# Kernel optimization log

Measured on AMD Instinct MI355X. Metric: run time of the kernel, lower is better.

The kernel has to match this reference:

```python
import jax, jax.numpy as jnp
import numpy as np
from jax import lax

H = 64      # hidden_size
VOC = 512   # num_embedding
L = 2       # num_layers


def layernorm(x, g, b, eps=1e-5):
    mu = jnp.mean(x, axis=-1, keepdims=True)
    var = jnp.mean((x - mu) ** 2, axis=-1, keepdims=True)
    return (x - mu) * lax.rsqrt(var + eps) * g + b


def conv3d(x, w, b):
    # x: [B, U, V, W, Cin] (channels-last), w: [3,3,3,Cin,Cout]
    return lax.conv_general_dilated(
        x, w, (1, 1, 1), 'SAME',
        dimension_numbers=('NDHWC', 'DHWIO', 'NDHWC')) + b


def setup_inputs() -> dict:
    key = jax.random.key(0)
    ks = jax.random.split(key, 8)
    f = lambda k, s, sc: jax.random.normal(k, s, jnp.float32) * sc
    return {
        'code': jax.random.randint(ks[0], (2, 5, 1, 8, 8, 8), 0, VOC),
        'ncode': jax.random.randint(ks[1], (2, 3, 1, 8, 8, 8), 0, VOC),
        'emb': f(ks[2], (VOC, H), 0.02),
        'win': f(ks[3], (L, 3, 3, 3, H, 4 * H), 0.05),
        'bin_': jnp.zeros((L, 4 * H), jnp.float32),
        'gin_w': jnp.ones((L, 4 * H), jnp.float32),
        'gin_b': jnp.zeros((L, 4 * H), jnp.float32),
        'wh': f(ks[4], (L, 3, 3, 3, H, 4 * H), 0.05),
        'bh': jnp.zeros((L, 4 * H), jnp.float32),
        'gh_w': jnp.ones((L, 4 * H), jnp.float32),
        'gh_b': jnp.zeros((L, 4 * H), jnp.float32),
        'w1': f(ks[5], (H, H), 0.05),
        'b1': jnp.zeros((H,), jnp.float32),
        'ln_g': jnp.ones((H,), jnp.float32),
        'ln_b': jnp.zeros((H,), jnp.float32),
        'w2': f(ks[6], (H, VOC), 0.05),
        'b2': jnp.zeros((VOC,), jnp.float32),
    }


def _forward(code, ncode, emb, win, bin_, gin_w, gin_b, wh, bh, gh_w, gh_b,
             w1, b1, ln_g, ln_b, w2, b2):
    N, Sn, C, U, V, W = ncode.shape
    x = jnp.concatenate([code, ncode[:, :-1]], axis=1)  # [N,S,C,U,V,W]
    S = x.shape[1]
    x = jnp.transpose(x, (0, 2, 1, 3, 4, 5)).reshape(N * C, S, U, V, W)
    h = emb[x]  # [NC, S, U, V, W, H]
    Hd = h.shape[-1]
    for i in range(L):
        # input-path conv is recurrence-free: batch it over all timesteps
        gi = layernorm(conv3d(h.reshape(N * C * S, U, V, W, Hd), win[i], bin_[i]),
                       gin_w[i], gin_b[i])
        gi = jnp.moveaxis(gi.reshape(N * C, S, U, V, W, 4 * Hd), 1, 0)  # [S,NC,U,V,W,4H]

        def step(carry, g, i=i):
            hx, cx = carry
            gates = g + layernorm(conv3d(hx, wh[i], bh[i]), gh_w[i], gh_b[i])
            ig, fg, cg, og = jnp.split(gates, 4, axis=-1)
            cx = jax.nn.sigmoid(fg) * cx + jax.nn.sigmoid(ig) * jnp.tanh(cg)
            hx = jax.nn.sigmoid(og) * jnp.tanh(cx)
            return (hx, cx), hx

        z = jnp.zeros((N * C, U, V, W, Hd), h.dtype)
        _, ys = lax.scan(step, (z, z), gi)
        h = jnp.moveaxis(ys, 0, 1)  # [NC,S,U,V,W,H]
    h = h[:, -Sn:].reshape(N, C, Sn, U, V, W, Hd)
    h = jnp.transpose(h, (0, 2, 1, 3, 4, 5, 6))  # [N,Sn,C,U,V,W,H]
    z = jax.nn.gelu(layernorm(h @ w1 + b1, ln_g, ln_b), approximate=False)
    logits = z @ w2 + b2  # [N,Sn,C,U,V,W,VOC]
    score = jnp.transpose(logits, (0, 6, 1, 2, 3, 4, 5))  # [N,VOC,Sn,C,U,V,W]
    logp = jax.nn.log_softmax(logits, axis=-1)
    loss = -jnp.mean(jnp.take_along_axis(logp, ncode[..., None], axis=-1))
    pred = jnp.argmax(score, axis=1)
    return score, loss, pred


def reference(code, ncode, emb, win, bin_, gin_w, gin_b, wh, bh, gh_w, gh_b,
              w1, b1, ln_g, ln_b, w2, b2):
    return _forward(code, ncode, emb, win, bin_, gin_w, gin_b, wh, bh,
                    gh_w, gh_b, w1, b1, ln_g, ln_b, w2, b2)
```

## Files before the change

kernel.cpp:

```cpp
#include <hip/hip_runtime.h>


typedef _Float16 f16;
typedef _Float16 f16x8 __attribute__((ext_vector_type(8)));
typedef float    f32x4 __attribute__((ext_vector_type(4)));

#define WSTRIDE 442368
#define WPT     884736
#define XSP     65536
#define HSP     458752
#define GPART   262144

__device__ __forceinline__ float wred_sum(float v) {
    #pragma unroll
    for (int o = 32; o > 0; o >>= 1) v += __shfl_down(v, o, 64);
    return __shfl(v, 0, 64);
}
__device__ __forceinline__ float fsig(float x)  { return 1.f / (1.f + __expf(-x)); }
__device__ __forceinline__ float ftanh(float x) { return 1.f - 2.f / (__expf(2.f*x) + 1.f); }

__global__ __launch_bounds__(256) void prep_kernel(
    const int* __restrict__ code, const int* __restrict__ ncode,
    const float* __restrict__ emb, f16* __restrict__ h,
    const float* __restrict__ win, const float* __restrict__ wh,
    f16* __restrict__ wp)
{
    if (blockIdx.x < 1792) {
        int e = blockIdx.x * 256 + threadIdx.x;
        int ch = e & 63;
        int pos = e >> 6;
        int vox = pos & 511;
        int t = pos >> 9;
        int s = t % 7, nc = t / 7;
        int tok = (s < 5) ? code[(nc*5 + s)*512 + vox]
                          : ncode[(nc*3 + (s-5))*512 + vox];
        float x = emb[tok*64 + ch];
        f16 hi = (f16)x;
        h[(size_t)pos*128 + ch]      = hi;
        h[(size_t)pos*128 + 64 + ch] = (f16)(x - (float)hi);
    } else {
        int b = blockIdx.x - 1792;
        int tensor = b / 27, tap = b % 27;
        const float* src = ((tensor & 1) ? wh : win) + (tensor >> 1) * WSTRIDE
                         + tap * 16384;
        int co = threadIdx.x;
        int sw = co & 7;
        #pragma unroll
        for (int hs = 0; hs < 2; ++hs) {
            f16* dst = wp + (((size_t)tensor*27 + tap)*2 + hs)*16384 + co*64;
            #pragma unroll
            for (int j = 0; j < 4; ++j) {
                f16x8 hi8, lo8;
                #pragma unroll
                for (int m = 0; m < 8; ++m) {
                    float w = src[(hs*32 + j*8 + m)*256 + co] * 64.f;
                    f16 hv = (f16)w;
                    hi8[m] = hv;
                    lo8[m] = (f16)(w - (float)hv);
                }
                *(f16x8*)(dst + ((j     ^ sw))*8) = hi8;
                *(f16x8*)(dst + (((4+j) ^ sw))*8) = lo8;
            }
        }
    }
}

struct MJob { const f16* x; const f16* w; float* y; };
struct MJobs { MJob j[8]; };

__global__ __launch_bounds__(256, 3) void conv_mfma_kernel(MJobs js)
{
    const MJob J = js.j[blockIdx.y];
    __shared__ float4 smem[2048];
    f16* wbuf = (f16*)smem;

    const int bx = blockIdx.x;
    const int cog = bx & 3, u = (bx >> 2) & 7, slab = (bx >> 5) & 1;
    const int ah = (bx >> 6) & 1, kb = bx >> 7;
    const int t = threadIdx.x, wid = t >> 6, l = t & 63;
    const int lv = (l >> 3) & 1, lw = l & 7, khi = l >> 4;

    const int gid = kb*4 + wid;
    const int g0  = (gid < 6) ? gid*7 : 42 + (gid - 6)*6;
    const int cnt = (gid < 6) ? 7 : 6;

    const f16* xbase = J.x + (size_t)slab * HSP;
    const f16* wjob  = J.w + (size_t)cog * 4096;
    f16* wmine = wbuf + wid * 4096;

    f16x8 wreg[8];
    auto wload = [&](int k) {
        const f16* src = wjob + (size_t)k * 16384 + l * 8;
        #pragma unroll
        for (int i = 0; i < 8; ++i) wreg[i] = *(const f16x8*)(src + i * 512);
    };
    auto wstore = [&]() {
        f16* dst = wmine + l * 8;
        #pragma unroll
        for (int i = 0; i < 8; ++i) *(f16x8*)(dst + i * 512) = wreg[i];
    };

    wload(g0); wstore();

    f32x4 acc[2][4] = {};
    for (int q = 0; q < cnt; ++q) {
        const int k = g0 + q;
        if (q + 1 < cnt) wload(k + 1);
        const int tap = k >> 1, hs = k & 1;
        const int du = tap / 9, rr = tap % 9, dv = rr / 3, dw = rr % 3;
        const int uu = u + du - 1;
        const bool uok = (unsigned)uu < 8u;
        const f16* xrow[2]; bool ok[2];
        #pragma unroll
        for (int aa = 0; aa < 2; ++aa) {
            int vs = (ah*2 + aa)*2 + lv + dv - 1, ws = lw + dw - 1;
            ok[aa] = uok && (unsigned)vs < 8u && (unsigned)ws < 8u;
            xrow[aa] = xbase + ((size_t)(uu*64 + vs*8 + ws) << 7) + khi*8;
        }
        const f16* wrow = wmine + (l & 15)*64;
        const int schi = ((khi    ) ^ lw) * 8;
        const int sclo = ((4 + khi) ^ lw) * 8;
        f16x8 ahi[2], alo[2], bhi[4], blo[4];
        #pragma unroll
        for (int aa = 0; aa < 2; ++aa) {
            f16x8 v = {0,0,0,0,0,0,0,0}, v2 = v;
            if (ok[aa]) {
                v  = *(const f16x8*)(xrow[aa] + hs*32);
                v2 = *(const f16x8*)(xrow[aa] + 64 + hs*32);
            }
            ahi[aa] = v; alo[aa] = v2;
        }
        #pragma unroll
        for (int n = 0; n < 4; ++n) {
            bhi[n] = *(const f16x8*)(wrow + n*1024 + schi);
            blo[n] = *(const f16x8*)(wrow + n*1024 + sclo);
        }
        #pragma unroll
        for (int aa = 0; aa < 2; ++aa)
            #pragma unroll
            for (int n = 0; n < 4; ++n)
                acc[aa][n] = __builtin_amdgcn_mfma_f32_16x16x32_f16(
                    ahi[aa], bhi[n], acc[aa][n], 0, 0, 0);
        #pragma unroll
        for (int aa = 0; aa < 2; ++aa)
            #pragma unroll
            for (int n = 0; n < 4; ++n)
                acc[aa][n] = __builtin_amdgcn_mfma_f32_16x16x32_f16(
                    alo[aa], bhi[n], acc[aa][n], 0, 0, 0);
        #pragma unroll
        for (int aa = 0; aa < 2; ++aa)
            #pragma unroll
            for (int n = 0; n < 4; ++n)
                acc[aa][n] = __builtin_amdgcn_mfma_f32_16x16x32_f16(
                    ahi[aa], blo[n], acc[aa][n], 0, 0, 0);
        if (q + 1 < cnt) wstore();
    }

    f32x4* red = (f32x4*)smem;
    {
        f32x4* mine = red + (size_t)(wid * 64 + l) * 8;
        #pragma unroll
        for (int aa = 0; aa < 2; ++aa)
            #pragma unroll
            for (int n = 0; n < 4; ++n)
                mine[(aa * 4 + n) ^ lw] = acc[aa][n];
    }
    __syncthreads();
    {
        float* yp = J.y + (size_t)kb * GPART;
        const int aa = (t >> 7) & 1, nsel = (t >> 6) & 1, ll = t & 63;
        #pragma unroll
        for (int ni = 0; ni < 2; ++ni) {
            const int n = nsel*2 + ni;
            const int ch = (aa * 4 + n) ^ (ll & 7);
            f32x4 sv = red[(0 * 64 + ll) * 8 + ch]
                     + red[(1 * 64 + ll) * 8 + ch]
                     + red[(2 * 64 + ll) * 8 + ch]
                     + red[(3 * 64 + ll) * 8 + ch];
            const int co = cog * 64 + n * 16 + (ll & 15);
            #pragma unroll
            for (int r = 0; r < 4; ++r) {
                int vox = (ah*2 + aa) * 16 + (ll >> 4) * 4 + r;
                yp[(size_t)(slab * 512 + u * 64 + vox) * 256 + co]
                    = sv[r] * 0.015625f;
            }
        }
    }
}

struct GJob {
    const float* giA; const float* giB;
    const float* ghA; const float* ghB;
    const float* bin; const float* bhb;
    const float* ginw; const float* ginb;
    const float* ghw;  const float* ghb;
    float* cx; f16* h16; int k; int k0;
};
__global__ __launch_bounds__(256) void gates_step_kernel(GJob ja, GJob jb)
{
    const GJob J = (blockIdx.y == 0) ? ja : jb;
    const int wid = threadIdx.x >> 6, lane = threadIdx.x & 63;
    const int row = blockIdx.x * 4 + wid;
    const int nc = row >> 9, vox = row & 511;

    const float* gA = J.giA + (size_t)row*256;
    const float* gB = J.giB + (size_t)row*256;
    float a0 = gA[lane]     + gB[lane]     + J.bin[lane];
    float a1 = gA[64+lane]  + gB[64+lane]  + J.bin[64+lane];
    float a2 = gA[128+lane] + gB[128+lane] + J.bin[128+lane];
    float a3 = gA[192+lane] + gB[192+lane] + J.bin[192+lane];
    float mu1 = wred_sum(a0+a1+a2+a3) * (1.f/256.f);
    float d0=a0-mu1, d1=a1-mu1, d2=a2-mu1, d3=a3-mu1;
    float v1 = wred_sum(d0*d0+d1*d1+d2*d2+d3*d3) * (1.f/256.f);
    float rs1 = rsqrtf(v1 + 1e-5f);

    float b0, b1, b2, b3;
    if (J.k0) {
        b0 = J.bhb[lane]; b1 = J.bhb[64+lane];
        b2 = J.bhb[128+lane]; b3 = J.bhb[192+lane];
    } else {
        const float* hA = J.ghA + (size_t)row*256;
        const float* hB = J.ghB + (size_t)row*256;
        b0 = hA[lane]     + hB[lane]     + J.bhb[lane];
        b1 = hA[64+lane]  + hB[64+lane]  + J.bhb[64+lane];
        b2 = hA[128+lane] + hB[128+lane] + J.bhb[128+lane];
        b3 = hA[192+lane] + hB[192+lane] + J.bhb[192+lane];
    }
    float mu2 = wred_sum(b0+b1+b2+b3) * (1.f/256.f);
    float e0=b0-mu2, e1=b1-mu2, e2=b2-mu2, e3=b3-mu2;
    float v2 = wred_sum(e0*e0+e1*e1+e2*e2+e3*e3) * (1.f/256.f);
    float rs2 = rsqrtf(v2 + 1e-5f);

    float Ig = d0*rs1*J.ginw[lane]     + J.ginb[lane]     + e0*rs2*J.ghw[lane]     + J.ghb[lane];
    float Fg = d1*rs1*J.ginw[64+lane]  + J.ginb[64+lane]  + e1*rs2*J.ghw[64+lane]  + J.ghb[64+lane];
    float Cg = d2*rs1*J.ginw[128+lane] + J.ginb[128+lane] + e2*rs2*J.ghw[128+lane] + J.ghb[128+lane];
    float Og = d3*rs1*J.ginw[192+lane] + J.ginb[192+lane] + e3*rs2*J.ghw[192+lane] + J.ghb[192+lane];

    float c_old = J.k0 ? 0.f : J.cx[(size_t)row*64 + lane];
    float c_new = fsig(Fg)*c_old + fsig(Ig)*ftanh(Cg);
    float h_new = fsig(Og)*ftanh(c_new);
    J.cx[(size_t)row*64 + lane] = c_new;
    size_t hb = ((size_t)(nc*7 + J.k)*512 + vox)*128 + lane;
    f16 hi = (f16)h_new;
    J.h16[hb]      = hi;
    J.h16[hb + 64] = (f16)(h_new - (float)hi);
}

__global__ __launch_bounds__(256) void head_kernel(
    const f16* __restrict__ h,
    const float* __restrict__ w1, const float* __restrict__ b1,
    const float* __restrict__ lng, const float* __restrict__ lnb,
    const float* __restrict__ w2, const float* __restrict__ b2,
    const int* __restrict__ ncode,
    float* __restrict__ out, float* __restrict__ lossb)
{
    __shared__ float hsm[4][64];
    __shared__ float zv[4][64];
    __shared__ float lg[4][512];
    __shared__ float lsum[4];
    const int blk = blockIdx.x;
    const int n = blk / 384;
    const int sn = (blk / 128) % 3;
    const int vox0 = (blk & 127) * 4;
    const int t = threadIdx.x, wid = t >> 6, lane = t & 63;
    const int vox = vox0 + wid;
    const f16* hv = h + (size_t)((n*7 + sn + 4)*512 + vox)*128;

    hsm[wid][lane] = (float)hv[lane] + (float)hv[64 + lane];

    float yva = b1[lane], yvb = 0.f;
    for (int kk = 0; kk < 64; kk += 2) {
        yva = fmaf(hsm[wid][kk],     w1[kk*64 + lane],     yva);
        yvb = fmaf(hsm[wid][kk + 1], w1[(kk+1)*64 + lane], yvb);
    }
    float yv = yva + yvb;
    float mu = wred_sum(yv) * (1.f/64.f);
    float d = yv - mu;
    float var = wred_sum(d*d) * (1.f/64.f);
    float ln = d * rsqrtf(var + 1e-5f) * lng[lane] + lnb[lane];
    zv[wid][lane] = 0.5f * ln * (1.f + erff(ln * 0.70710678118654752f));

    float l[8];
    #pragma unroll
    for (int j = 0; j < 8; ++j) l[j] = b2[j*64 + lane];
    for (int kk = 0; kk < 64; ++kk) {
        float zz = zv[wid][kk];
        #pragma unroll
        for (int j = 0; j < 8; ++j)
            l[j] = fmaf(zz, w2[kk*512 + j*64 + lane], l[j]);
    }
    #pragma unroll
    for (int j = 0; j < 8; ++j) lg[wid][j*64 + lane] = l[j];

    float m = l[0]; int mi = lane;
    #pragma unroll
    for (int j = 1; j < 8; ++j)
        if (l[j] > m) { m = l[j]; mi = j*64 + lane; }
    #pragma unroll
    for (int o = 32; o > 0; o >>= 1) {
        float om = __shfl_down(m, o, 64);
        int   oi = __shfl_down(mi, o, 64);
        if (om > m || (om == m && oi < mi)) { m = om; mi = oi; }
    }
    float maxv = __shfl(m, 0, 64);
    int   maxi = __shfl(mi, 0, 64);
    float es = 0.f;
    #pragma unroll
    for (int j = 0; j < 8; ++j) es += __expf(l[j] - maxv);
    float sum = wred_sum(es);
    if (lane == 0) {
        int target = ncode[(n*3 + sn)*512 + vox];
        float logp = lg[wid][target] - maxv - __logf(sum);
        lsum[wid] = -logp * (1.f/3072.f);
        out[1572865 + (n*3 + sn)*512 + vox] = (float)maxi;
    }

    __syncthreads();
    if (t == 0) lossb[blk] = lsum[0] + lsum[1] + lsum[2] + lsum[3];
    for (int co = t; co < 512; co += 256) {
        float4 o4 = { lg[0][co], lg[1][co], lg[2][co], lg[3][co] };
        *(float4*)(out + (size_t)((n*512 + co)*3 + sn)*512 + vox0) = o4;
    }
}

__global__ void loss_fin_kernel(const float* __restrict__ lossb,
                                float* __restrict__ out)
{
    float s = 0.f;
    for (int i = threadIdx.x; i < 768; i += 64) s += lossb[i];
    s = wred_sum(s);
    if (threadIdx.x == 0) out[1572864] = s;
}

extern "C" void kernel_launch(void* const* d_in, const int* in_sizes, int n_in,
                              void* d_out, int out_size, void* d_ws, size_t ws_size,
                              hipStream_t stream) {
    (void)in_sizes; (void)n_in; (void)out_size; (void)ws_size;
    const int*   code  = (const int*)d_in[0];
    const int*   ncode = (const int*)d_in[1];
    const float* emb   = (const float*)d_in[2];
    const float* win   = (const float*)d_in[3];
    const float* bin_  = (const float*)d_in[4];
    const float* gin_w = (const float*)d_in[5];
    const float* gin_b = (const float*)d_in[6];
    const float* wh    = (const float*)d_in[7];
    const float* bh    = (const float*)d_in[8];
    const float* gh_w  = (const float*)d_in[9];
    const float* gh_b  = (const float*)d_in[10];
    const float* w1    = (const float*)d_in[11];
    const float* b1    = (const float*)d_in[12];
    const float* ln_g  = (const float*)d_in[13];
    const float* ln_b  = (const float*)d_in[14];
    const float* w2    = (const float*)d_in[15];
    const float* b2    = (const float*)d_in[16];
    float* out = (float*)d_out;

    float* base  = (float*)d_ws;
    f16*   wp    = (f16*)base;
    f16*   h1    = (f16*)(base + 1769472);
    f16*   h2    = (f16*)(base + 2228224);
    float* gi1   = base + 2686976;
    float* gi2   = gi1 + 7*2*(size_t)GPART;
    float* ghat1 = gi2 + 2*GPART;
    float* ghat2 = ghat1 + 2*GPART;
    float* cx1   = ghat2 + 2*GPART;
    float* cx2   = cx1 + 65536;
    float* lossb = base + 8060928;

    const f16* win0 = wp;
    const f16* wh0  = wp + WPT;
    const f16* win1 = wp + 2*WPT;
    const f16* wh1  = wp + 3*WPT;

    prep_kernel<<<1900, 256, 0, stream>>>(code, ncode, emb, h1, win, wh, wp);

    {
        MJobs js{};
        for (int s = 0; s < 7; ++s)
            js.j[s] = { h1 + (size_t)s*XSP, win0, gi1 + (size_t)s*2*GPART };
        conv_mfma_kernel<<<dim3(256, 7), 256, 0, stream>>>(js);
    }

    for (int s = 0; s <= 7; ++s) {
        GJob g1 = { gi1 + (size_t)s*2*GPART, gi1 + (size_t)s*2*GPART + GPART,
                    ghat1, ghat1 + GPART, bin_, bh,
                    gin_w, gin_b, gh_w, gh_b, cx1, h1, s, s == 0 };
        GJob g2 = { gi2, gi2 + GPART, ghat2, ghat2 + GPART, bin_ + 256, bh + 256,
                    gin_w + 256, gin_b + 256, gh_w + 256, gh_b + 256,
                    cx2, h2, s - 1, s == 1 };
        if (s == 0)
            gates_step_kernel<<<dim3(256, 1), 256, 0, stream>>>(g1, g1);
        else if (s <= 6)
            gates_step_kernel<<<dim3(256, 2), 256, 0, stream>>>(g1, g2);
        else
            gates_step_kernel<<<dim3(256, 1), 256, 0, stream>>>(g2, g2);

        MJobs js{}; int nj = 0;
        if (s <= 5) js.j[nj++] = { h1 + (size_t)s*XSP,     wh0,  ghat1 };
        if (s <= 6) js.j[nj++] = { h1 + (size_t)s*XSP,     win1, gi2 };
        if (s >= 1 && s <= 6)
                    js.j[nj++] = { h2 + (size_t)(s-1)*XSP, wh1,  ghat2 };
        if (nj > 0)
            conv_mfma_kernel<<<dim3(256, nj), 256, 0, stream>>>(js);
    }

    head_kernel<<<768, 256, 0, stream>>>(h2, w1, b1, ln_g, ln_b, w2, b2,
                                         ncode, out, lossb);
    loss_fin_kernel<<<1, 64, 0, stream>>>(lossb, out);
}
```

Before: 305.7 us.

## Gather embeddings inside first conv and fuse final gate step into head

The prep kernel now builds only a split-f16 copy of the embedding table, not the full per-timestep hidden tensor. The first input-path conv gathers rows from that table by token index. The last layer-2 LSTM gate step is folded into the head kernel for the final timestep, which removes one kernel launch and a round trip of h through memory. The conv kernel's launch bounds occupancy hint also goes from 3 to 4 blocks per SM. In exchange, the conv inner loop gets a dependent token load and a branch, and the extra register pressure may cause spills.

```diff
diff --git a/kernel.cpp b/kernel.cpp
--- a/kernel.cpp
+++ b/kernel.cpp
@@ -20,26 +20,12 @@
 __device__ __forceinline__ float ftanh(float x) { return 1.f - 2.f / (__expf(2.f*x) + 1.f); }
 
 __global__ __launch_bounds__(256) void prep_kernel(
-    const int* __restrict__ code, const int* __restrict__ ncode,
-    const float* __restrict__ emb, f16* __restrict__ h,
+    const float* __restrict__ emb, f16* __restrict__ emb16,
     const float* __restrict__ win, const float* __restrict__ wh,
     f16* __restrict__ wp)
 {
-    if (blockIdx.x < 1792) {
-        int e = blockIdx.x * 256 + threadIdx.x;
-        int ch = e & 63;
-        int pos = e >> 6;
-        int vox = pos & 511;
-        int t = pos >> 9;
-        int s = t % 7, nc = t / 7;
-        int tok = (s < 5) ? code[(nc*5 + s)*512 + vox]
-                          : ncode[(nc*3 + (s-5))*512 + vox];
-        float x = emb[tok*64 + ch];
-        f16 hi = (f16)x;
-        h[(size_t)pos*128 + ch]      = hi;
-        h[(size_t)pos*128 + 64 + ch] = (f16)(x - (float)hi);
-    } else {
-        int b = blockIdx.x - 1792;
+    if (blockIdx.x < 108) {
+        int b = blockIdx.x;
         int tensor = b / 27, tap = b % 27;
         const float* src = ((tensor & 1) ? wh : win) + (tensor >> 1) * WSTRIDE
                          + tap * 16384;
@@ -62,13 +48,21 @@
                 *(f16x8*)(dst + (((4+j) ^ sw))*8) = lo8;
             }
         }
-    }
-}
-
-struct MJob { const f16* x; const f16* w; float* y; };
+    } else {
+        int e = (blockIdx.x - 108) * 256 + threadIdx.x;
+        int ch = e & 63, tok = e >> 6;
+        float x = emb[tok*64 + ch];
+        f16 hi = (f16)x;
+        emb16[tok*128 + ch]      = hi;
+        emb16[tok*128 + 64 + ch] = (f16)(x - (float)hi);
+    }
+}
+
+struct MJob { const f16* x; const f16* w; float* y;
+              const int* toks; int tokStride; };
 struct MJobs { MJob j[8]; };
 
-__global__ __launch_bounds__(256, 3) void conv_mfma_kernel(MJobs js)
+__global__ __launch_bounds__(256, 4) void conv_mfma_kernel(MJobs js)
 {
     const MJob J = js.j[blockIdx.y];
     __shared__ float4 smem[2048];
@@ -84,7 +78,9 @@
     const int g0  = (gid < 6) ? gid*7 : 42 + (gid - 6)*6;
     const int cnt = (gid < 6) ? 7 : 6;
 
-    const f16* xbase = J.x + (size_t)slab * HSP;
+    const bool gather = (J.toks != nullptr);
+    const f16* xbase = J.x + (gather ? 0 : (size_t)slab * HSP);
+    const int* tbase = gather ? (J.toks + slab * J.tokStride) : nullptr;
     const f16* wjob  = J.w + (size_t)cog * 4096;
     f16* wmine = wbuf + wid * 4096;
 
@@ -115,7 +111,14 @@
         for (int aa = 0; aa < 2; ++aa) {
             int vs = (ah*2 + aa)*2 + lv + dv - 1, ws = lw + dw - 1;
             ok[aa] = uok && (unsigned)vs < 8u && (unsigned)ws < 8u;
-            xrow[aa] = xbase + ((size_t)(uu*64 + vs*8 + ws) << 7) + khi*8;
+            int voxidx = uu*64 + vs*8 + ws;
+            if (gather) {
+                int tok = 0;
+                if (ok[aa]) tok = tbase[voxidx];
+                xrow[aa] = xbase + (size_t)tok*128 + khi*8;
+            } else {
+                xrow[aa] = xbase + ((size_t)voxidx << 7) + khi*8;
+            }
         }
         const f16* wrow = wmine + (l & 15)*64;
         const int schi = ((khi    ) ^ lw) * 8;
@@ -252,7 +255,7 @@
     const float* __restrict__ lng, const float* __restrict__ lnb,
     const float* __restrict__ w2, const float* __restrict__ b2,
     const int* __restrict__ ncode,
-    float* __restrict__ out, float* __restrict__ lossb)
+    float* __restrict__ out, float* __restrict__ lossb, GJob g2)
 {
     __shared__ float hsm[4][64];
     __shared__ float zv[4][64];
@@ -264,9 +267,43 @@
     const int vox0 = (blk & 127) * 4;
     const int t = threadIdx.x, wid = t >> 6, lane = t & 63;
     const int vox = vox0 + wid;
-    const f16* hv = h + (size_t)((n*7 + sn + 4)*512 + vox)*128;
-
-    hsm[wid][lane] = (float)hv[lane] + (float)hv[64 + lane];
+
+    if (sn == 2) {
+        const int row = n*512 + vox;
+        const float* gA = g2.giA + (size_t)row*256;
+        const float* gB = g2.giB + (size_t)row*256;
+        float a0 = gA[lane]     + gB[lane]     + g2.bin[lane];
+        float a1 = gA[64+lane]  + gB[64+lane]  + g2.bin[64+lane];
+        float a2 = gA[128+lane] + gB[128+lane] + g2.bin[128+lane];
+        float a3 = gA[192+lane] + gB[192+lane] + g2.bin[192+lane];
+        float mu1 = wred_sum(a0+a1+a2+a3) * (1.f/256.f);
+        float d0=a0-mu1, d1=a1-mu1, d2=a2-mu1, d3=a3-mu1;
+        float v1 = wred_sum(d0*d0+d1*d1+d2*d2+d3*d3) * (1.f/256.f);
+        float rs1 = rsqrtf(v1 + 1e-5f);
+
+        const float* hA = g2.ghA + (size_t)row*256;
+        const float* hB = g2.ghB + (size_t)row*256;
+        float b0v = hA[lane]     + hB[lane]     + g2.bhb[lane];
+        float b1v = hA[64+lane]  + hB[64+lane]  + g2.bhb[64+lane];
+        float b2v = hA[128+lane] + hB[128+lane] + g2.bhb[128+lane];
+        float b3v = hA[192+lane] + hB[192+lane] + g2.bhb[192+lane];
+        float mu2 = wred_sum(b0v+b1v+b2v+b3v) * (1.f/256.f);
+        float e0=b0v-mu2, e1=b1v-mu2, e2=b2v-mu2, e3=b3v-mu2;
+        float v2 = wred_sum(e0*e0+e1*e1+e2*e2+e3*e3) * (1.f/256.f);
+        float rs2 = rsqrtf(v2 + 1e-5f);
+
+        float Ig = d0*rs1*g2.ginw[lane]     + g2.ginb[lane]     + e0*rs2*g2.ghw[lane]     + g2.ghb[lane];
+        float Fg = d1*rs1*g2.ginw[64+lane]  + g2.ginb[64+lane]  + e1*rs2*g2.ghw[64+lane]  + g2.ghb[64+lane];
+        float Cg = d2*rs1*g2.ginw[128+lane] + g2.ginb[128+lane] + e2*rs2*g2.ghw[128+lane] + g2.ghb[128+lane];
+        float Og = d3*rs1*g2.ginw[192+lane] + g2.ginb[192+lane] + e3*rs2*g2.ghw[192+lane] + g2.ghb[192+lane];
+
+        float c_old = g2.cx[(size_t)row*64 + lane];
+        float c_new = fsig(Fg)*c_old + fsig(Ig)*ftanh(Cg);
+        hsm[wid][lane] = fsig(Og)*ftanh(c_new);
+    } else {
+        const f16* hv = h + (size_t)((n*7 + sn + 4)*512 + vox)*128;
+        hsm[wid][lane] = (float)hv[lane] + (float)hv[64 + lane];
+    }
 
     float yva = b1[lane], yvb = 0.f;
     for (int kk = 0; kk < 64; kk += 2) {
@@ -357,31 +394,37 @@
 
     float* base  = (float*)d_ws;
     f16*   wp    = (f16*)base;
-    f16*   h1    = (f16*)(base + 1769472);
-    f16*   h2    = (f16*)(base + 2228224);
-    float* gi1   = base + 2686976;
+    f16*   emb16 = (f16*)(base + 1769472);
+    f16*   h1    = (f16*)(base + 1802240);
+    f16*   h2    = (f16*)(base + 2260992);
+    float* gi1   = base + 2719744;
     float* gi2   = gi1 + 7*2*(size_t)GPART;
     float* ghat1 = gi2 + 2*GPART;
     float* ghat2 = ghat1 + 2*GPART;
     float* cx1   = ghat2 + 2*GPART;
     float* cx2   = cx1 + 65536;
-    float* lossb = base + 8060928;
+    float* lossb = base + 8093696;
 
     const f16* win0 = wp;
     const f16* wh0  = wp + WPT;
     const f16* win1 = wp + 2*WPT;
     const f16* wh1  = wp + 3*WPT;
 
-    prep_kernel<<<1900, 256, 0, stream>>>(code, ncode, emb, h1, win, wh, wp);
+    prep_kernel<<<236, 256, 0, stream>>>(emb, emb16, win, wh, wp);
 
     {
         MJobs js{};
-        for (int s = 0; s < 7; ++s)
-            js.j[s] = { h1 + (size_t)s*XSP, win0, gi1 + (size_t)s*2*GPART };
+        for (int s = 0; s < 7; ++s) {
+            MJob j;
+            j.x = emb16; j.w = win0; j.y = gi1 + (size_t)s*2*GPART;
+            if (s < 5) { j.toks = code + s*512;        j.tokStride = 5*512; }
+            else       { j.toks = ncode + (s-5)*512;   j.tokStride = 3*512; }
+            js.j[s] = j;
+        }
         conv_mfma_kernel<<<dim3(256, 7), 256, 0, stream>>>(js);
     }
 
-    for (int s = 0; s <= 7; ++s) {
+    for (int s = 0; s <= 6; ++s) {
         GJob g1 = { gi1 + (size_t)s*2*GPART, gi1 + (size_t)s*2*GPART + GPART,
                     ghat1, ghat1 + GPART, bin_, bh,
                     gin_w, gin_b, gh_w, gh_b, cx1, h1, s, s == 0 };
@@ -390,21 +433,20 @@
                     cx2, h2, s - 1, s == 1 };
         if (s == 0)
             gates_step_kernel<<<dim3(256, 1), 256, 0, stream>>>(g1, g1);
-        else if (s <= 6)
+        else
             gates_step_kernel<<<dim3(256, 2), 256, 0, stream>>>(g1, g2);
-        else
-            gates_step_kernel<<<dim3(256, 1), 256, 0, stream>>>(g2, g2);
 
         MJobs js{}; int nj = 0;
-        if (s <= 5) js.j[nj++] = { h1 + (size_t)s*XSP,     wh0,  ghat1 };
-        if (s <= 6) js.j[nj++] = { h1 + (size_t)s*XSP,     win1, gi2 };
-        if (s >= 1 && s <= 6)
-                    js.j[nj++] = { h2 + (size_t)(s-1)*XSP, wh1,  ghat2 };
-        if (nj > 0)
-            conv_mfma_kernel<<<dim3(256, nj), 256, 0, stream>>>(js);
-    }
-
+        if (s <= 5) js.j[nj++] = { h1 + (size_t)s*XSP,     wh0,  ghat1, nullptr, 0 };
+        js.j[nj++]             = { h1 + (size_t)s*XSP,     win1, gi2,   nullptr, 0 };
+        if (s >= 1) js.j[nj++] = { h2 + (size_t)(s-1)*XSP, wh1,  ghat2, nullptr, 0 };
+        conv_mfma_kernel<<<dim3(256, nj), 256, 0, stream>>>(js);
+    }
+
+    GJob g2h = { gi2, gi2 + GPART, ghat2, ghat2 + GPART, bin_ + 256, bh + 256,
+                 gin_w + 256, gin_b + 256, gh_w + 256, gh_b + 256,
+                 cx2, h2, 6, 0 };
     head_kernel<<<768, 256, 0, stream>>>(h2, w1, b1, ln_g, ln_b, w2, b2,
-                                         ncode, out, lossb);
+                                         ncode, out, lossb, g2h);
     loss_fin_kernel<<<1, 64, 0, stream>>>(lossb, out);
 }
```

After: 304.4 us. Within noise of the previous version (-0.4%).

## Split conv K-reduction four ways and fuse final LSTM gate step into head

Applied to the files above, without the earlier changes.

The conv kernel's 27-tap by two-half reduction is now split across four partial-sum slices instead of two. The grid doubles to 512 blocks per job and occupancy is raised to 4 blocks per CU, aiming to fill the GPU better on the small per-step launches. The gates kernel and the new head path sum four partials, which increases partial-buffer traffic. The last layer-2 gate step is folded into the head kernel for the final timestep, removing one launch from the serial chain.

```diff
diff --git a/kernel.cpp b/kernel.cpp
--- a/kernel.cpp
+++ b/kernel.cpp
@@ -68,7 +68,7 @@
 struct MJob { const f16* x; const f16* w; float* y; };
 struct MJobs { MJob j[8]; };
 
-__global__ __launch_bounds__(256, 3) void conv_mfma_kernel(MJobs js)
+__global__ __launch_bounds__(256, 4) void conv_mfma_kernel(MJobs js)
 {
     const MJob J = js.j[blockIdx.y];
     __shared__ float4 smem[2048];
@@ -81,8 +81,8 @@
     const int lv = (l >> 3) & 1, lw = l & 7, khi = l >> 4;
 
     const int gid = kb*4 + wid;
-    const int g0  = (gid < 6) ? gid*7 : 42 + (gid - 6)*6;
-    const int cnt = (gid < 6) ? 7 : 6;
+    const int g0  = (gid < 6) ? gid*4 : 24 + (gid - 6)*3;
+    const int cnt = (gid < 6) ? 4 : 3;
 
     const f16* xbase = J.x + (size_t)slab * HSP;
     const f16* wjob  = J.w + (size_t)cog * 4096;
@@ -189,8 +189,8 @@
 }
 
 struct GJob {
-    const float* giA; const float* giB;
-    const float* ghA; const float* ghB;
+    const float* gi;
+    const float* gh;
     const float* bin; const float* bhb;
     const float* ginw; const float* ginb;
     const float* ghw;  const float* ghb;
@@ -203,12 +203,15 @@
     const int row = blockIdx.x * 4 + wid;
     const int nc = row >> 9, vox = row & 511;
 
-    const float* gA = J.giA + (size_t)row*256;
-    const float* gB = J.giB + (size_t)row*256;
-    float a0 = gA[lane]     + gB[lane]     + J.bin[lane];
-    float a1 = gA[64+lane]  + gB[64+lane]  + J.bin[64+lane];
-    float a2 = gA[128+lane] + gB[128+lane] + J.bin[128+lane];
-    float a3 = gA[192+lane] + gB[192+lane] + J.bin[192+lane];
+    const float* g = J.gi + (size_t)row*256;
+    float a0 = g[lane]             + g[GPART+lane]
+             + g[2*GPART+lane]     + g[3*GPART+lane]     + J.bin[lane];
+    float a1 = g[64+lane]          + g[GPART+64+lane]
+             + g[2*GPART+64+lane]  + g[3*GPART+64+lane]  + J.bin[64+lane];
+    float a2 = g[128+lane]         + g[GPART+128+lane]
+             + g[2*GPART+128+lane] + g[3*GPART+128+lane] + J.bin[128+lane];
+    float a3 = g[192+lane]         + g[GPART+192+lane]
+             + g[2*GPART+192+lane] + g[3*GPART+192+lane] + J.bin[192+lane];
     float mu1 = wred_sum(a0+a1+a2+a3) * (1.f/256.f);
     float d0=a0-mu1, d1=a1-mu1, d2=a2-mu1, d3=a3-mu1;
     float v1 = wred_sum(d0*d0+d1*d1+d2*d2+d3*d3) * (1.f/256.f);
@@ -219,12 +222,15 @@
         b0 = J.bhb[lane]; b1 = J.bhb[64+lane];
         b2 = J.bhb[128+lane]; b3 = J.bhb[192+lane];
     } else {
-        const float* hA = J.ghA + (size_t)row*256;
-        const float* hB = J.ghB + (size_t)row*256;
-        b0 = hA[lane]     + hB[lane]     + J.bhb[lane];
-        b1 = hA[64+lane]  + hB[64+lane]  + J.bhb[64+lane];
-        b2 = hA[128+lane] + hB[128+lane] + J.bhb[128+lane];
-        b3 = hA[192+lane] + hB[192+lane] + J.bhb[192+lane];
+        const float* hh = J.gh + (size_t)row*256;
+        b0 = hh[lane]             + hh[GPART+lane]
+           + hh[2*GPART+lane]     + hh[3*GPART+lane]     + J.bhb[lane];
+        b1 = hh[64+lane]          + hh[GPART+64+lane]
+           + hh[2*GPART+64+lane]  + hh[3*GPART+64+lane]  + J.bhb[64+lane];
+        b2 = hh[128+lane]         + hh[GPART+128+lane]
+           + hh[2*GPART+128+lane] + hh[3*GPART+128+lane] + J.bhb[128+lane];
+        b3 = hh[192+lane]         + hh[GPART+192+lane]
+           + hh[2*GPART+192+lane] + hh[3*GPART+192+lane] + J.bhb[192+lane];
     }
     float mu2 = wred_sum(b0+b1+b2+b3) * (1.f/256.f);
     float e0=b0-mu2, e1=b1-mu2, e2=b2-mu2, e3=b3-mu2;
@@ -252,7 +258,7 @@
     const float* __restrict__ lng, const float* __restrict__ lnb,
     const float* __restrict__ w2, const float* __restrict__ b2,
     const int* __restrict__ ncode,
-    float* __restrict__ out, float* __restrict__ lossb)
+    float* __restrict__ out, float* __restrict__ lossb, GJob g2)
 {
     __shared__ float hsm[4][64];
     __shared__ float zv[4][64];
@@ -264,9 +270,49 @@
     const int vox0 = (blk & 127) * 4;
     const int t = threadIdx.x, wid = t >> 6, lane = t & 63;
     const int vox = vox0 + wid;
-    const f16* hv = h + (size_t)((n*7 + sn + 4)*512 + vox)*128;
-
-    hsm[wid][lane] = (float)hv[lane] + (float)hv[64 + lane];
+
+    if (sn == 2) {
+        const int row = n*512 + vox;
+        const float* g = g2.gi + (size_t)row*256;
+        float a0 = g[lane]             + g[GPART+lane]
+                 + g[2*GPART+lane]     + g[3*GPART+lane]     + g2.bin[lane];
+        float a1 = g[64+lane]          + g[GPART+64+lane]
+                 + g[2*GPART+64+lane]  + g[3*GPART+64+lane]  + g2.bin[64+lane];
+        float a2 = g[128+lane]         + g[GPART+128+lane]
+                 + g[2*GPART+128+lane] + g[3*GPART+128+lane] + g2.bin[128+lane];
+        float a3 = g[192+lane]         + g[GPART+192+lane]
+                 + g[2*GPART+192+lane] + g[3*GPART+192+lane] + g2.bin[192+lane];
+        float mu1 = wred_sum(a0+a1+a2+a3) * (1.f/256.f);
+        float d0=a0-mu1, d1=a1-mu1, d2=a2-mu1, d3=a3-mu1;
+        float v1 = wred_sum(d0*d0+d1*d1+d2*d2+d3*d3) * (1.f/256.f);
+        float rs1 = rsqrtf(v1 + 1e-5f);
+
+        const float* hh = g2.gh + (size_t)row*256;
+        float b0v = hh[lane]             + hh[GPART+lane]
+                  + hh[2*GPART+lane]     + hh[3*GPART+lane]     + g2.bhb[lane];
+        float b1v = hh[64+lane]          + hh[GPART+64+lane]
+                  + hh[2*GPART+64+lane]  + hh[3*GPART+64+lane]  + g2.bhb[64+lane];
+        float b2v = hh[128+lane]         + hh[GPART+128+lane]
+                  + hh[2*GPART+128+lane] + hh[3*GPART+128+lane] + g2.bhb[128+lane];
+        float b3v = hh[192+lane]         + hh[GPART+192+lane]
+                  + hh[2*GPART+192+lane] + hh[3*GPART+192+lane] + g2.bhb[192+lane];
+        float mu2 = wred_sum(b0v+b1v+b2v+b3v) * (1.f/256.f);
+        float e0=b0v-mu2, e1=b1v-mu2, e2=b2v-mu2, e3=b3v-mu2;
+        float v2 = wred_sum(e0*e0+e1*e1+e2*e2+e3*e3) * (1.f/256.f);
+        float rs2 = rsqrtf(v2 + 1e-5f);
+
+        float Ig = d0*rs1*g2.ginw[lane]     + g2.ginb[lane]     + e0*rs2*g2.ghw[lane]     + g2.ghb[lane];
+        float Fg = d1*rs1*g2.ginw[64+lane]  + g2.ginb[64+lane]  + e1*rs2*g2.ghw[64+lane]  + g2.ghb[64+lane];
+        float Cg = d2*rs1*g2.ginw[128+lane] + g2.ginb[128+lane] + e2*rs2*g2.ghw[128+lane] + g2.ghb[128+lane];
+        float Og = d3*rs1*g2.ginw[192+lane] + g2.ginb[192+lane] + e3*rs2*g2.ghw[192+lane] + g2.ghb[192+lane];
+
+        float c_old = g2.cx[(size_t)row*64 + lane];
+        float c_new = fsig(Fg)*c_old + fsig(Ig)*ftanh(Cg);
+        hsm[wid][lane] = fsig(Og)*ftanh(c_new);
+    } else {
+        const f16* hv = h + (size_t)((n*7 + sn + 4)*512 + vox)*128;
+        hsm[wid][lane] = (float)hv[lane] + (float)hv[64 + lane];
+    }
 
     float yva = b1[lane], yvb = 0.f;
     for (int kk = 0; kk < 64; kk += 2) {
@@ -360,12 +406,12 @@
     f16*   h1    = (f16*)(base + 1769472);
     f16*   h2    = (f16*)(base + 2228224);
     float* gi1   = base + 2686976;
-    float* gi2   = gi1 + 7*2*(size_t)GPART;
-    float* ghat1 = gi2 + 2*GPART;
-    float* ghat2 = ghat1 + 2*GPART;
-    float* cx1   = ghat2 + 2*GPART;
+    float* gi2   = gi1 + 7*4*(size_t)GPART;
+    float* ghat1 = gi2 + 4*(size_t)GPART;
+    float* ghat2 = ghat1 + 4*(size_t)GPART;
+    float* cx1   = ghat2 + 4*(size_t)GPART;
     float* cx2   = cx1 + 65536;
-    float* lossb = base + 8060928;
+    float* lossb = base + 13303808;
 
     const f16* win0 = wp;
     const f16* wh0  = wp + WPT;
@@ -377,34 +423,32 @@
     {
         MJobs js{};
         for (int s = 0; s < 7; ++s)
-            js.j[s] = { h1 + (size_t)s*XSP, win0, gi1 + (size_t)s*2*GPART };
-        conv_mfma_kernel<<<dim3(256, 7), 256, 0, stream>>>(js);
-    }
-
-    for (int s = 0; s <= 7; ++s) {
-        GJob g1 = { gi1 + (size_t)s*2*GPART, gi1 + (size_t)s*2*GPART + GPART,
-                    ghat1, ghat1 + GPART, bin_, bh,
+            js.j[s] = { h1 + (size_t)s*XSP, win0, gi1 + (size_t)s*4*GPART };
+        conv_mfma_kernel<<<dim3(512, 7), 256, 0, stream>>>(js);
+    }
+
+    for (int s = 0; s <= 6; ++s) {
+        GJob g1 = { gi1 + (size_t)s*4*GPART, ghat1, bin_, bh,
                     gin_w, gin_b, gh_w, gh_b, cx1, h1, s, s == 0 };
-        GJob g2 = { gi2, gi2 + GPART, ghat2, ghat2 + GPART, bin_ + 256, bh + 256,
+        GJob g2 = { gi2, ghat2, bin_ + 256, bh + 256,
                     gin_w + 256, gin_b + 256, gh_w + 256, gh_b + 256,
                     cx2, h2, s - 1, s == 1 };
         if (s == 0)
             gates_step_kernel<<<dim3(256, 1), 256, 0, stream>>>(g1, g1);
-        else if (s <= 6)
+        else
             gates_step_kernel<<<dim3(256, 2), 256, 0, stream>>>(g1, g2);
-        else
-            gates_step_kernel<<<dim3(256, 1), 256, 0, stream>>>(g2, g2);
 
         MJobs js{}; int nj = 0;
         if (s <= 5) js.j[nj++] = { h1 + (size_t)s*XSP,     wh0,  ghat1 };
-        if (s <= 6) js.j[nj++] = { h1 + (size_t)s*XSP,     win1, gi2 };
-        if (s >= 1 && s <= 6)
-                    js.j[nj++] = { h2 + (size_t)(s-1)*XSP, wh1,  ghat2 };
-        if (nj > 0)
-            conv_mfma_kernel<<<dim3(256, nj), 256, 0, stream>>>(js);
-    }
-
+        js.j[nj++]             = { h1 + (size_t)s*XSP,     win1, gi2 };
+        if (s >= 1) js.j[nj++] = { h2 + (size_t)(s-1)*XSP, wh1,  ghat2 };
+        conv_mfma_kernel<<<dim3(512, nj), 256, 0, stream>>>(js);
+    }
+
+    GJob g2h = { gi2, ghat2, bin_ + 256, bh + 256,
+                 gin_w + 256, gin_b + 256, gh_w + 256, gh_b + 256,
+                 cx2, h2, 6, 0 };
     head_kernel<<<768, 256, 0, stream>>>(h2, w1, b1, ln_g, ln_b, w2, b2,
-                                         ncode, out, lossb);
+                                         ncode, out, lossb, g2h);
     loss_fin_kernel<<<1, 64, 0, stream>>>(lossb, out);
 }
```

Measured after the change: 311.1 us. Within noise of the previous version (+1.8%).

## Use channel-blocked f16 activation layout and fuse last LSTM step into head

Applied to the files above, without the earlier changes.

Activations move from a per-voxel [vox][hi64|lo64] layout to a channel-blocked [chgroup][vox][8] layout, so each conv A-operand load reads contiguous voxels within a channel group. The final layer-2 gate step is computed inside the head kernel for the last timestep, which removes one gates launch and the store and reload of that hidden state. Conv launch bounds are raised to 4 waves per SIMD, which may force register spills.

```diff
diff --git a/kernel.cpp b/kernel.cpp
--- a/kernel.cpp
+++ b/kernel.cpp
@@ -30,14 +30,15 @@
         int ch = e & 63;
         int pos = e >> 6;
         int vox = pos & 511;
-        int t = pos >> 9;
-        int s = t % 7, nc = t / 7;
+        int slab = pos >> 9;
+        int s = slab % 7, nc = slab / 7;
         int tok = (s < 5) ? code[(nc*5 + s)*512 + vox]
                           : ncode[(nc*3 + (s-5))*512 + vox];
         float x = emb[tok*64 + ch];
         f16 hi = (f16)x;
-        h[(size_t)pos*128 + ch]      = hi;
-        h[(size_t)pos*128 + 64 + ch] = (f16)(x - (float)hi);
+        size_t sb = (size_t)slab * XSP;
+        h[sb + (ch>>3)*4096       + vox*8 + (ch&7)] = hi;
+        h[sb + ((ch>>3)+8)*4096   + vox*8 + (ch&7)] = (f16)(x - (float)hi);
     } else {
         int b = blockIdx.x - 1792;
         int tensor = b / 27, tap = b % 27;
@@ -68,7 +69,7 @@
 struct MJob { const f16* x; const f16* w; float* y; };
 struct MJobs { MJob j[8]; };
 
-__global__ __launch_bounds__(256, 3) void conv_mfma_kernel(MJobs js)
+__global__ __launch_bounds__(256, 4) void conv_mfma_kernel(MJobs js)
 {
     const MJob J = js.j[blockIdx.y];
     __shared__ float4 smem[2048];
@@ -110,12 +111,13 @@
         const int du = tap / 9, rr = tap % 9, dv = rr / 3, dw = rr % 3;
         const int uu = u + du - 1;
         const bool uok = (unsigned)uu < 8u;
+        const int choff = (khi + hs*4) * 4096;
         const f16* xrow[2]; bool ok[2];
         #pragma unroll
         for (int aa = 0; aa < 2; ++aa) {
             int vs = (ah*2 + aa)*2 + lv + dv - 1, ws = lw + dw - 1;
             ok[aa] = uok && (unsigned)vs < 8u && (unsigned)ws < 8u;
-            xrow[aa] = xbase + ((size_t)(uu*64 + vs*8 + ws) << 7) + khi*8;
+            xrow[aa] = xbase + choff + (uu*64 + vs*8 + ws)*8;
         }
         const f16* wrow = wmine + (l & 15)*64;
         const int schi = ((khi    ) ^ lw) * 8;
@@ -125,8 +127,8 @@
         for (int aa = 0; aa < 2; ++aa) {
             f16x8 v = {0,0,0,0,0,0,0,0}, v2 = v;
             if (ok[aa]) {
-                v  = *(const f16x8*)(xrow[aa] + hs*32);
-                v2 = *(const f16x8*)(xrow[aa] + 64 + hs*32);
+                v  = *(const f16x8*)(xrow[aa]);
+                v2 = *(const f16x8*)(xrow[aa] + 32768);
             }
             ahi[aa] = v; alo[aa] = v2;
         }
@@ -240,10 +242,10 @@
     float c_new = fsig(Fg)*c_old + fsig(Ig)*ftanh(Cg);
     float h_new = fsig(Og)*ftanh(c_new);
     J.cx[(size_t)row*64 + lane] = c_new;
-    size_t hb = ((size_t)(nc*7 + J.k)*512 + vox)*128 + lane;
+    size_t sb = (size_t)(nc*7 + J.k) * XSP;
     f16 hi = (f16)h_new;
-    J.h16[hb]      = hi;
-    J.h16[hb + 64] = (f16)(h_new - (float)hi);
+    J.h16[sb + (lane>>3)*4096     + vox*8 + (lane&7)] = hi;
+    J.h16[sb + ((lane>>3)+8)*4096 + vox*8 + (lane&7)] = (f16)(h_new - (float)hi);
 }
 
 __global__ __launch_bounds__(256) void head_kernel(
@@ -252,7 +254,7 @@
     const float* __restrict__ lng, const float* __restrict__ lnb,
     const float* __restrict__ w2, const float* __restrict__ b2,
     const int* __restrict__ ncode,
-    float* __restrict__ out, float* __restrict__ lossb)
+    float* __restrict__ out, float* __restrict__ lossb, GJob g2)
 {
     __shared__ float hsm[4][64];
     __shared__ float zv[4][64];
@@ -264,9 +266,44 @@
     const int vox0 = (blk & 127) * 4;
     const int t = threadIdx.x, wid = t >> 6, lane = t & 63;
     const int vox = vox0 + wid;
-    const f16* hv = h + (size_t)((n*7 + sn + 4)*512 + vox)*128;
-
-    hsm[wid][lane] = (float)hv[lane] + (float)hv[64 + lane];
+
+    if (sn == 2) {
+        const int row = n*512 + vox;
+        const float* gA = g2.giA + (size_t)row*256;
+        const float* gB = g2.giB + (size_t)row*256;
+        float a0 = gA[lane]     + gB[lane]     + g2.bin[lane];
+        float a1 = gA[64+lane]  + gB[64+lane]  + g2.bin[64+lane];
+        float a2 = gA[128+lane] + gB[128+lane] + g2.bin[128+lane];
+        float a3 = gA[192+lane] + gB[192+lane] + g2.bin[192+lane];
+        float mu1 = wred_sum(a0+a1+a2+a3) * (1.f/256.f);
+        float d0=a0-mu1, d1=a1-mu1, d2=a2-mu1, d3=a3-mu1;
+        float v1 = wred_sum(d0*d0+d1*d1+d2*d2+d3*d3) * (1.f/256.f);
+        float rs1 = rsqrtf(v1 + 1e-5f);
+
+        const float* hA = g2.ghA + (size_t)row*256;
+        const float* hB = g2.ghB + (size_t)row*256;
+        float b0v = hA[lane]     + hB[lane]     + g2.bhb[lane];
+        float b1v = hA[64+lane]  + hB[64+lane]  + g2.bhb[64+lane];
+        float b2v = hA[128+lane] + hB[128+lane] + g2.bhb[128+lane];
+        float b3v = hA[192+lane] + hB[192+lane] + g2.bhb[192+lane];
+        float mu2 = wred_sum(b0v+b1v+b2v+b3v) * (1.f/256.f);
+        float e0=b0v-mu2, e1=b1v-mu2, e2=b2v-mu2, e3=b3v-mu2;
+        float v2 = wred_sum(e0*e0+e1*e1+e2*e2+e3*e3) * (1.f/256.f);
+        float rs2 = rsqrtf(v2 + 1e-5f);
+
+        float Ig = d0*rs1*g2.ginw[lane]     + g2.ginb[lane]     + e0*rs2*g2.ghw[lane]     + g2.ghb[lane];
+        float Fg = d1*rs1*g2.ginw[64+lane]  + g2.ginb[64+lane]  + e1*rs2*g2.ghw[64+lane]  + g2.ghb[64+lane];
+        float Cg = d2*rs1*g2.ginw[128+lane] + g2.ginb[128+lane] + e2*rs2*g2.ghw[128+lane] + g2.ghb[128+lane];
+        float Og = d3*rs1*g2.ginw[192+lane] + g2.ginb[192+lane] + e3*rs2*g2.ghw[192+lane] + g2.ghb[192+lane];
+
+        float c_old = g2.cx[(size_t)row*64 + lane];
+        float c_new = fsig(Fg)*c_old + fsig(Ig)*ftanh(Cg);
+        hsm[wid][lane] = fsig(Og)*ftanh(c_new);
+    } else {
+        const f16* hv = h + (size_t)(n*7 + sn + 4) * XSP;
+        hsm[wid][lane] = (float)hv[(lane>>3)*4096     + vox*8 + (lane&7)]
+                       + (float)hv[((lane>>3)+8)*4096 + vox*8 + (lane&7)];
+    }
 
     float yva = b1[lane], yvb = 0.f;
     for (int kk = 0; kk < 64; kk += 2) {
@@ -381,7 +418,7 @@
         conv_mfma_kernel<<<dim3(256, 7), 256, 0, stream>>>(js);
     }
 
-    for (int s = 0; s <= 7; ++s) {
+    for (int s = 0; s <= 6; ++s) {
         GJob g1 = { gi1 + (size_t)s*2*GPART, gi1 + (size_t)s*2*GPART + GPART,
                     ghat1, ghat1 + GPART, bin_, bh,
                     gin_w, gin_b, gh_w, gh_b, cx1, h1, s, s == 0 };
@@ -390,21 +427,20 @@
                     cx2, h2, s - 1, s == 1 };
         if (s == 0)
             gates_step_kernel<<<dim3(256, 1), 256, 0, stream>>>(g1, g1);
-        else if (s <= 6)
+        else
             gates_step_kernel<<<dim3(256, 2), 256, 0, stream>>>(g1, g2);
-        else
-            gates_step_kernel<<<dim3(256, 1), 256, 0, stream>>>(g2, g2);
 
         MJobs js{}; int nj = 0;
         if (s <= 5) js.j[nj++] = { h1 + (size_t)s*XSP,     wh0,  ghat1 };
-        if (s <= 6) js.j[nj++] = { h1 + (size_t)s*XSP,     win1, gi2 };
-        if (s >= 1 && s <= 6)
-                    js.j[nj++] = { h2 + (size_t)(s-1)*XSP, wh1,  ghat2 };
-        if (nj > 0)
-            conv_mfma_kernel<<<dim3(256, nj), 256, 0, stream>>>(js);
-    }
-
+        js.j[nj++]             = { h1 + (size_t)s*XSP,     win1, gi2 };
+        if (s >= 1) js.j[nj++] = { h2 + (size_t)(s-1)*XSP, wh1,  ghat2 };
+        conv_mfma_kernel<<<dim3(256, nj), 256, 0, stream>>>(js);
+    }
+
+    GJob g2h = { gi2, gi2 + GPART, ghat2, ghat2 + GPART, bin_ + 256, bh + 256,
+                 gin_w + 256, gin_b + 256, gh_w + 256, gh_b + 256,
+                 cx2, h2, 6, 0 };
     head_kernel<<<768, 256, 0, stream>>>(h2, w1, b1, ln_g, ln_b, w2, b2,
-                                         ncode, out, lossb);
+                                         ncode, out, lossb, g2h);
     loss_fin_kernel<<<1, 64, 0, stream>>>(lossb, out);
 }
```

Result: faster. 279.3 us (-8.6%).
